# Kernel optimization log

Measured on AMD Instinct MI355X. Metric: run time of the kernel, lower is better.

The kernel has to match this reference:

```python
import jax, jax.numpy as jnp
import numpy as np

# irreps '32x0e + 32x1o + 16x2e': dims 32 (l=0), 96 (l=1, 32x3), 80 (l=2, 16x5) -> 208
MUL0, MUL1, MUL2 = 32, 32, 16
SC = 64  # scalar_channels
N_NODES, N_EDGES = 50000, 200000
FAN_IN = MUL0 * MUL0 + MUL1 * MUL1 + MUL2 * MUL2  # fully-connected path fan-in


def setup_inputs() -> dict:
    key = jax.random.key(0)
    ks = jax.random.split(key, 10)
    node_tensors = jax.random.normal(ks[0], (N_NODES, 208), dtype=jnp.float32)
    edge_index = jax.random.randint(ks[1], (2, N_EDGES), 0, N_NODES)
    # FullyConnectedTensorProduct path weights (mul1, mul2, mul_out)
    W0 = jax.random.normal(ks[2], (MUL0, MUL0, SC), dtype=jnp.float32)
    W1 = jax.random.normal(ks[3], (MUL1, MUL1, SC), dtype=jnp.float32)
    W2 = jax.random.normal(ks[4], (MUL2, MUL2, SC), dtype=jnp.float32)
    # MLP: Linear(64,32) -> SiLU -> Linear(32,1)
    A1 = jax.random.normal(ks[5], (SC, SC // 2), dtype=jnp.float32) / np.float32(np.sqrt(SC))
    b1 = jnp.zeros((SC // 2,), dtype=jnp.float32)
    A2 = jax.random.normal(ks[6], (SC // 2, 1), dtype=jnp.float32) / np.float32(np.sqrt(SC // 2))
    b2 = jnp.zeros((1,), dtype=jnp.float32)
    return {"node_tensors": node_tensors, "edge_index": edge_index,
            "W0": W0, "W1": W1, "W2": W2, "A1": A1, "b1": b1, "A2": A2, "b2": b2}


def _split_irreps(x):
    # x: [E, 208] -> scalars [E,32], vectors [E,32,3], rank-2 [E,16,5]
    s = x[:, :MUL0]
    v = x[:, MUL0:MUL0 + MUL1 * 3].reshape(-1, MUL1, 3)
    t = x[:, MUL0 + MUL1 * 3:].reshape(-1, MUL2, 5)
    return s, v, t


def reference(node_tensors, edge_index, W0, W1, W2, A1, b1, A2, b2):
    src, dst = edge_index[0], edge_index[1]
    x1 = node_tensors[src]  # [E, 208]
    x2 = node_tensors[dst]
    s1, v1, t1 = _split_irreps(x1)
    s2, v2, t2 = _split_irreps(x2)
    alpha = np.float32(1.0 / np.sqrt(FAN_IN))  # path normalization
    # l x l -> 0 Clebsch-Gordan: delta_{m1 m2} / sqrt(2l+1)
    e = alpha * (
        jnp.einsum('eu,ev,uvw->ew', s1, s2, W0)
        + jnp.einsum('eum,evm,uvw->ew', v1, v2, W1) / np.float32(np.sqrt(3.0))
        + jnp.einsum('eum,evm,uvw->ew', t1, t2, W2) / np.float32(np.sqrt(5.0))
    )  # [E, 64]
    h = jax.nn.silu(e @ A1 + b1)
    return (h @ A2 + b2)[:, 0]  # [E]
```

## Files before the change

kernel.cpp:

```cpp
#include <hip/hip_runtime.h>
#include <hip/hip_fp16.h>
#include <stdint.h>

#define N_EDGES 200000
#define N_NODES 50000
#define BM 32
#define NT 64

typedef _Float16 f16x8 __attribute__((ext_vector_type(8)));
typedef float f32x4 __attribute__((ext_vector_type(4)));

__global__ void prep_w(const float* __restrict__ W0, const float* __restrict__ W1,
                       const float* __restrict__ W2, uint16_t* __restrict__ wt) {
  int o = blockIdx.x * 256 + threadIdx.x;
  int T = o >> 11, r = o & 2047, w = r >> 5, kk = r & 31;
  int k = T * 32 + kk;
  const float AS = 1.0f / 48.0f;
  const float AV = AS * 0.57735026918962576f;
  const float AT = AS * 0.44721359549995794f;
  float val;
  if (k < 1024)      val = AS * W0[(k >> 5) * 2048 + (k & 31) * 64 + w];
  else if (k < 2048) { int k2 = k - 1024; val = AV * W1[(k2 >> 5) * 2048 + (k2 & 31) * 64 + w]; }
  else               { int k2 = k - 2048; val = AT * W2[(k2 >> 4) * 1024 + (k2 & 15) * 64 + w]; }
  __half h = __float2half(val);
  wt[o] = *reinterpret_cast<uint16_t*>(&h);
}

__global__ void prep_tables(const float* __restrict__ nt,
                            uint16_t* __restrict__ ta, uint16_t* __restrict__ tb) {
  long long o = (long long)blockIdx.x * 256 + threadIdx.x;
  if (o >= (long long)N_NODES * 296) return;
  int node = (int)(o / 296);
  int r = (int)(o - (long long)node * 296);
  const float* x = nt + (size_t)node * 208;
  float va = 0.f;
  if (r < 32) va = x[r];
  else if (r < 160) { int q = r - 32;  int u = q >> 2, m = q & 3;  if (m < 3) va = x[32 + u * 3 + m]; }
  else if (r < 288) { int q = r - 160; int u = q >> 3, m = q & 7;  if (m < 5) va = x[128 + u * 5 + m]; }
  __half ha = __float2half(va);
  ta[(size_t)node * 296 + r] = *reinterpret_cast<uint16_t*>(&ha);
  if (r < 216) {
    float vb = 0.f;
    if (r < 32) vb = x[r];
    else if (r < 128) { int q = r - 32;  int m = q >> 5, v = q & 31; vb = x[32 + v * 3 + m]; }
    else if (r < 208) { int q = r - 128; int m = q >> 4, v = q & 15; vb = x[128 + v * 5 + m]; }
    __half hb = __float2half(vb);
    tb[(size_t)node * 216 + r] = *reinterpret_cast<uint16_t*>(&hb);
  }
}

__device__ __forceinline__ __half2 bcast_half(uint32_t w, int sel) {
  uint32_t hv = sel ? (w >> 16) : (w & 0xffffu);
  hv |= hv << 16;
  union { uint32_t u; __half2 h; } cv; cv.u = hv;
  return cv.h;
}

#define LOADW(WRA, TEXPR)                                                       \
  { int Tc_ = (TEXPR);                                                          \
    _Pragma("unroll") for (int nf = 0; nf < 4; ++nf)                            \
      WRA[nf] = wtg4[Tc_ * 256 + nf * 64 + lo4]; }

#define MSTEPA(WRA, A)                                                          \
  _Pragma("unroll") for (int mf = 0; mf < 2; ++mf)                              \
  _Pragma("unroll") for (int nf = 0; nf < 4; ++nf)                              \
    acc[mf][nf] = __builtin_amdgcn_mfma_f32_16x16x32_f16(                       \
        (A)[mf], *(const f16x8*)&WRA[nf], acc[mf][nf], 0, 0, 0);

#define BUILD_SR(T_, A)                                                         \
  _Pragma("unroll") for (int mf = 0; mf < 2; ++mf) {                            \
    __half2 s1b2 = bcast_half(sS[mf][(T_) >> 1], (T_) & 1);                     \
    union { uint32_t u[4]; f16x8 v; } au_;                                      \
    _Pragma("unroll") for (int q = 0; q < 4; ++q) {                             \
      __half2 p = __hmul2(s1b2, ((const __half2*)&s2pk[mf])[q]);                \
      au_.u[q] = *(uint32_t*)&p;                                                \
    }                                                                           \
    (A)[mf] = au_.v;                                                            \
  }

#define BUILD_VR(UL, A)                                                         \
  _Pragma("unroll") for (int mf = 0; mf < 2; ++mf) {                            \
    __half2 va0 = bcast_half(vS[mf][(UL) * 2], 0);                              \
    __half2 va1 = bcast_half(vS[mf][(UL) * 2], 1);                              \
    __half2 va2 = bcast_half(vS[mf][(UL) * 2 + 1], 0);                          \
    union { uint32_t u[4]; f16x8 v; } au_;                                      \
    _Pragma("unroll") for (int q = 0; q < 4; ++q) {                             \
      __half2 p = __hmul2(va0, ((const __half2*)&v2pk[mf][0])[q]);              \
      p = __hfma2(va1, ((const __half2*)&v2pk[mf][1])[q], p);                   \
      p = __hfma2(va2, ((const __half2*)&v2pk[mf][2])[q], p);                   \
      au_.u[q] = *(uint32_t*)&p;                                                \
    }                                                                           \
    (A)[mf] = au_.v;                                                            \
  }

#define BUILD_TR(TT_, A)                                                        \
  _Pragma("unroll") for (int mm = 0; mm < 2; ++mm) {                            \
    __half2 tb0 = bcast_half(tS[mm][(TT_) * 4 + 0], 0);                         \
    __half2 tb1 = bcast_half(tS[mm][(TT_) * 4 + 0], 1);                         \
    __half2 tb2 = bcast_half(tS[mm][(TT_) * 4 + 1], 0);                         \
    __half2 tb3 = bcast_half(tS[mm][(TT_) * 4 + 1], 1);                         \
    __half2 tb4 = bcast_half(tS[mm][(TT_) * 4 + 2], 0);                         \
    union { uint32_t u[4]; f16x8 v; } au_;                                      \
    _Pragma("unroll") for (int q = 0; q < 4; ++q) {                             \
      __half2 p = __hmul2(tb0, ((const __half2*)&t2pk[mm][0])[q]);              \
      p = __hfma2(tb1, ((const __half2*)&t2pk[mm][1])[q], p);                   \
      p = __hfma2(tb2, ((const __half2*)&t2pk[mm][2])[q], p);                   \
      p = __hfma2(tb3, ((const __half2*)&t2pk[mm][3])[q], p);                   \
      p = __hfma2(tb4, ((const __half2*)&t2pk[mm][4])[q], p);                   \
      au_.u[q] = *(uint32_t*)&p;                                                \
    }                                                                           \
    (A)[mm] = au_.v;                                                            \
  }

#define RING_SR(WRA, T_)     { f16x8 a[2]; BUILD_SR(T_, a); MSTEPA(WRA, a); LOADW(WRA, (T_) + 4); }
#define RING_VR(WRA, UL, TB) { f16x8 a[2]; BUILD_VR(UL, a); MSTEPA(WRA, a); LOADW(WRA, (TB) + (UL) + 4); }
#define WRAPT(X) ((X) <= 71 ? (X) : (X) - 8)
#define RING_TR(WRA, TT_, TB){ f16x8 a[2]; BUILD_TR(TT_, a); MSTEPA(WRA, a); LOADW(WRA, WRAPT((TB) + (TT_) + 4)); }

__global__ __launch_bounds__(NT) void edge_main(
    const uint16_t* __restrict__ ta, const uint16_t* __restrict__ tbl,
    const int* __restrict__ ei, const uint16_t* __restrict__ wt,
    const float* __restrict__ A1, const float* __restrict__ b1,
    const float* __restrict__ A2, const float* __restrict__ b2,
    float* __restrict__ out)
{
  __shared__ alignas(16) float etile[32 * 68];
  const int tid = threadIdx.x;
  const int e0 = blockIdx.x * BM;
  const int lane = tid, c = lane & 15, g = lane >> 4;
  const int lo4 = c * 4 + g;

  const unsigned char* x1p[2];
  const unsigned char* tbp[2];
  #pragma unroll
  for (int mf = 0; mf < 2; ++mf) {
    int e = e0 + mf * 16 + c;
    int src = ei[e];
    int dst = ei[N_EDGES + e];
    x1p[mf] = (const unsigned char*)ta + (size_t)src * 592;
    tbp[mf] = (const unsigned char*)tbl + (size_t)dst * 432;
  }

  f32x4 acc[2][4];
  #pragma unroll
  for (int mf = 0; mf < 2; ++mf)
    #pragma unroll
    for (int nf = 0; nf < 4; ++nf) acc[mf][nf] = (f32x4){0.f, 0.f, 0.f, 0.f};

  const uint4* wtg4 = (const uint4*)wt;
  uint4 wr0[4], wr1[4], wr2[4], wr3[4];
  LOADW(wr0, 0); LOADW(wr1, 1); LOADW(wr2, 2); LOADW(wr3, 3);

  {
    uint4 s2pk[2];
    #pragma unroll
    for (int mf = 0; mf < 2; ++mf) s2pk[mf] = *(const uint4*)(tbp[mf] + g * 16);
    uint32_t sS[2][16];
    #pragma unroll
    for (int mf = 0; mf < 2; ++mf)
      #pragma unroll
      for (int i = 0; i < 4; ++i) {
        uint4 q_ = *(const uint4*)(x1p[mf] + i * 16);
        sS[mf][i * 4 + 0] = q_.x; sS[mf][i * 4 + 1] = q_.y;
        sS[mf][i * 4 + 2] = q_.z; sS[mf][i * 4 + 3] = q_.w;
      }
    #pragma unroll
    for (int T4 = 0; T4 < 8; ++T4) {
      RING_SR(wr0, T4 * 4 + 0); RING_SR(wr1, T4 * 4 + 1);
      RING_SR(wr2, T4 * 4 + 2); RING_SR(wr3, T4 * 4 + 3);
    }
  }

  {
    uint4 v2pk[2][3];
    #pragma unroll
    for (int mf = 0; mf < 2; ++mf)
      #pragma unroll
      for (int m3 = 0; m3 < 3; ++m3)
        v2pk[mf][m3] = *(const uint4*)(tbp[mf] + 64 + m3 * 64 + g * 16);
    for (int G = 0; G < 4; ++G) {
      uint32_t vS[2][16];
      #pragma unroll
      for (int mf = 0; mf < 2; ++mf)
        #pragma unroll
        for (int i = 0; i < 4; ++i) {
          uint4 q_ = *(const uint4*)(x1p[mf] + 64 + G * 64 + i * 16);
          vS[mf][i * 4 + 0] = q_.x; vS[mf][i * 4 + 1] = q_.y;
          vS[mf][i * 4 + 2] = q_.z; vS[mf][i * 4 + 3] = q_.w;
        }
      const int Tb = 32 + G * 8;
      RING_VR(wr0, 0, Tb); RING_VR(wr1, 1, Tb); RING_VR(wr2, 2, Tb); RING_VR(wr3, 3, Tb);
      RING_VR(wr0, 4, Tb); RING_VR(wr1, 5, Tb); RING_VR(wr2, 6, Tb); RING_VR(wr3, 7, Tb);
    }
  }

  {
    uint4 t2pk[2][5];
    #pragma unroll
    for (int mm = 0; mm < 2; ++mm)
      #pragma unroll
      for (int m5 = 0; m5 < 5; ++m5)
        t2pk[mm][m5] = *(const uint4*)(tbp[mm] + 256 + m5 * 32 + (g & 1) * 16);
    const int gh16 = (g >> 1) * 16;
    #pragma unroll
    for (int H = 0; H < 2; ++H) {
      uint32_t tS[2][16];
      #pragma unroll
      for (int mm = 0; mm < 2; ++mm)
        #pragma unroll
        for (int i = 0; i < 4; ++i) {
          uint4 q_ = *(const uint4*)(x1p[mm] + 320 + gh16 + H * 128 + i * 32);
          tS[mm][i * 4 + 0] = q_.x; tS[mm][i * 4 + 1] = q_.y;
          tS[mm][i * 4 + 2] = q_.z; tS[mm][i * 4 + 3] = q_.w;
        }
      const int Tb = 64 + H * 4;
      RING_TR(wr0, 0, Tb); RING_TR(wr1, 1, Tb); RING_TR(wr2, 2, Tb); RING_TR(wr3, 3, Tb);
    }
  }

  #pragma unroll
  for (int mf = 0; mf < 2; ++mf)
    #pragma unroll
    for (int nf = 0; nf < 4; ++nf)
      #pragma unroll
      for (int rr = 0; rr < 4; ++rr)
        etile[(mf * 16 + g * 4 + rr) * 68 + nf * 16 + c] = acc[mf][nf][rr];
  __syncthreads();

  {
    int el = lane >> 1, jh = lane & 1;
    const float* er = etile + (size_t)el * 68;
    float hacc[16];
    #pragma unroll
    for (int j = 0; j < 16; ++j) hacc[j] = b1[jh * 16 + j];
    for (int w4 = 0; w4 < 16; ++w4) {
      float4 ea = *(const float4*)(er + w4 * 4);
      #pragma unroll
      for (int q2 = 0; q2 < 4; ++q2) {
        float ev = (&ea.x)[q2];
        int w = w4 * 4 + q2;
        float4 a0 = *(const float4*)(A1 + w * 32 + jh * 16);
        float4 a1 = *(const float4*)(A1 + w * 32 + jh * 16 + 4);
        float4 a2 = *(const float4*)(A1 + w * 32 + jh * 16 + 8);
        float4 a3 = *(const float4*)(A1 + w * 32 + jh * 16 + 12);
        hacc[0]  += ev * a0.x; hacc[1]  += ev * a0.y; hacc[2]  += ev * a0.z; hacc[3]  += ev * a0.w;
        hacc[4]  += ev * a1.x; hacc[5]  += ev * a1.y; hacc[6]  += ev * a1.z; hacc[7]  += ev * a1.w;
        hacc[8]  += ev * a2.x; hacc[9]  += ev * a2.y; hacc[10] += ev * a2.z; hacc[11] += ev * a2.w;
        hacc[12] += ev * a3.x; hacc[13] += ev * a3.y; hacc[14] += ev * a3.z; hacc[15] += ev * a3.w;
      }
    }
    float o = 0.f;
    #pragma unroll
    for (int j = 0; j < 16; ++j) {
      float z = hacc[j];
      o += (z / (1.f + __expf(-z))) * A2[jh * 16 + j];
    }
    o += __shfl_xor(o, 1);
    int e = e0 + el;
    if (jh == 0 && e < N_EDGES) out[e] = o + b2[0];
  }
}

extern "C" void kernel_launch(void* const* d_in, const int* in_sizes, int n_in,
                              void* d_out, int out_size, void* d_ws, size_t ws_size,
                              hipStream_t stream) {
  const float* nt = (const float*)d_in[0];
  const int*   ei = (const int*)d_in[1];
  const float* W0 = (const float*)d_in[2];
  const float* W1 = (const float*)d_in[3];
  const float* W2 = (const float*)d_in[4];
  const float* A1 = (const float*)d_in[5];
  const float* b1 = (const float*)d_in[6];
  const float* A2 = (const float*)d_in[7];
  const float* b2 = (const float*)d_in[8];
  float* out = (float*)d_out;

  uint16_t* wt = (uint16_t*)d_ws;
  uint16_t* ta = (uint16_t*)((char*)d_ws + 294912);
  uint16_t* tb = (uint16_t*)((char*)d_ws + 294912 + (size_t)N_NODES * 592);

  prep_w<<<576, 256, 0, stream>>>(W0, W1, W2, wt);
  {
    long long tot = (long long)N_NODES * 296;
    int blocks = (int)((tot + 255) / 256);
    prep_tables<<<blocks, 256, 0, stream>>>(nt, ta, tb);
  }
  edge_main<<<N_EDGES / BM, NT, 0, stream>>>(ta, tb, ei, wt, A1, b1, A2, b2, out);
}
```

Measured before the change: 226.6 us.

## Stage shared fp16 weights through LDS with async global-to-LDS ring buffer

```diff
diff --git a/kernel.cpp b/kernel.cpp
--- a/kernel.cpp
+++ b/kernel.cpp
@@ -4,8 +4,9 @@
 
 #define N_EDGES 200000
 #define N_NODES 50000
-#define BM 32
-#define NT 64
+#define BM 256
+#define NT 512
+#define GTOT 36
 
 typedef _Float16 f16x8 __attribute__((ext_vector_type(8)));
 typedef float f32x4 __attribute__((ext_vector_type(4)));
@@ -49,6 +50,12 @@
   }
 }
 
+__device__ __forceinline__ void gload16(const void* g, void* l) {
+  __builtin_amdgcn_global_load_lds(
+      (const __attribute__((address_space(1))) void*)g,
+      (__attribute__((address_space(3))) void*)l, 16, 0, 0);
+}
+
 __device__ __forceinline__ __half2 bcast_half(uint32_t w, int sel) {
   uint32_t hv = sel ? (w >> 16) : (w & 0xffffu);
   hv |= hv << 16;
@@ -56,10 +63,23 @@
   return cv.h;
 }
 
-#define LOADW(WRA, TEXPR)                                                       \
-  { int Tc_ = (TEXPR);                                                          \
+#define STAGEW(G)                                                               \
+  if ((G) < GTOT) {                                                             \
+    gload16((const char*)wt + (size_t)(G) * 8192 + tid * 16,                    \
+            (void*)(smem + ((G) & 3) * 8192 + (tid >> 6) * 1024));              \
+  }
+#define WAITV(G)                                                                \
+  do {                                                                          \
+    if ((G) >= GTOT - 1)      asm volatile("s_waitcnt vmcnt(0)" ::: "memory");  \
+    else if ((G) == GTOT - 2) asm volatile("s_waitcnt vmcnt(1)" ::: "memory");  \
+    else                      asm volatile("s_waitcnt vmcnt(2)" ::: "memory");  \
+  } while (0)
+#define BARRIER() asm volatile("s_barrier" ::: "memory")
+
+#define LDSW(WRA, G, TL)                                                        \
+  { const uint4* wb_ = (const uint4*)(smem + ((G) & 3) * 8192 + (TL) * 4096);   \
     _Pragma("unroll") for (int nf = 0; nf < 4; ++nf)                            \
-      WRA[nf] = wtg4[Tc_ * 256 + nf * 64 + lo4]; }
+      WRA[nf] = wb_[nf * 64 + lo4]; }
 
 #define MSTEPA(WRA, A)                                                          \
   _Pragma("unroll") for (int mf = 0; mf < 2; ++mf)                              \
@@ -112,29 +132,26 @@
     (A)[mm] = au_.v;                                                            \
   }
 
-#define RING_SR(WRA, T_)     { f16x8 a[2]; BUILD_SR(T_, a); MSTEPA(WRA, a); LOADW(WRA, (T_) + 4); }
-#define RING_VR(WRA, UL, TB) { f16x8 a[2]; BUILD_VR(UL, a); MSTEPA(WRA, a); LOADW(WRA, (TB) + (UL) + 4); }
-#define WRAPT(X) ((X) <= 71 ? (X) : (X) - 8)
-#define RING_TR(WRA, TT_, TB){ f16x8 a[2]; BUILD_TR(TT_, a); MSTEPA(WRA, a); LOADW(WRA, WRAPT((TB) + (TT_) + 4)); }
-
-__global__ __launch_bounds__(NT) void edge_main(
+__global__ __launch_bounds__(NT, 2) void edge_main(
     const uint16_t* __restrict__ ta, const uint16_t* __restrict__ tbl,
     const int* __restrict__ ei, const uint16_t* __restrict__ wt,
     const float* __restrict__ A1, const float* __restrict__ b1,
     const float* __restrict__ A2, const float* __restrict__ b2,
     float* __restrict__ out)
 {
-  __shared__ alignas(16) float etile[32 * 68];
+  __shared__ alignas(16) unsigned char smem[69632];
   const int tid = threadIdx.x;
   const int e0 = blockIdx.x * BM;
-  const int lane = tid, c = lane & 15, g = lane >> 4;
+  const int lane = tid & 63, c = lane & 15, g = lane >> 4;
+  const int wv = tid >> 6;
   const int lo4 = c * 4 + g;
 
   const unsigned char* x1p[2];
   const unsigned char* tbp[2];
   #pragma unroll
   for (int mf = 0; mf < 2; ++mf) {
-    int e = e0 + mf * 16 + c;
+    int e = e0 + wv * 32 + mf * 16 + c;
+    if (e > N_EDGES - 1) e = N_EDGES - 1;
     int src = ei[e];
     int dst = ei[N_EDGES + e];
     x1p[mf] = (const unsigned char*)ta + (size_t)src * 592;
@@ -147,9 +164,8 @@
     #pragma unroll
     for (int nf = 0; nf < 4; ++nf) acc[mf][nf] = (f32x4){0.f, 0.f, 0.f, 0.f};
 
-  const uint4* wtg4 = (const uint4*)wt;
-  uint4 wr0[4], wr1[4], wr2[4], wr3[4];
-  LOADW(wr0, 0); LOADW(wr1, 1); LOADW(wr2, 2); LOADW(wr3, 3);
+  STAGEW(0);
+  STAGEW(1);
 
   {
     uint4 s2pk[2];
@@ -165,9 +181,14 @@
         sS[mf][i * 4 + 2] = q_.z; sS[mf][i * 4 + 3] = q_.w;
       }
     #pragma unroll
-    for (int T4 = 0; T4 < 8; ++T4) {
-      RING_SR(wr0, T4 * 4 + 0); RING_SR(wr1, T4 * 4 + 1);
-      RING_SR(wr2, T4 * 4 + 2); RING_SR(wr3, T4 * 4 + 3);
+    for (int q = 0; q < 16; ++q) {
+      STAGEW(q + 2);
+      WAITV(q);
+      BARRIER();
+      uint4 wrA[4], wrB[4];
+      LDSW(wrA, q, 0); LDSW(wrB, q, 1);
+      { f16x8 a[2]; BUILD_SR(2 * q, a);     MSTEPA(wrA, a); }
+      { f16x8 a[2]; BUILD_SR(2 * q + 1, a); MSTEPA(wrB, a); }
     }
   }
 
@@ -178,19 +199,27 @@
       #pragma unroll
       for (int m3 = 0; m3 < 3; ++m3)
         v2pk[mf][m3] = *(const uint4*)(tbp[mf] + 64 + m3 * 64 + g * 16);
-    for (int G = 0; G < 4; ++G) {
-      uint32_t vS[2][16];
-      #pragma unroll
-      for (int mf = 0; mf < 2; ++mf)
+    uint32_t vS[2][16];
+    #pragma unroll
+    for (int q = 0; q < 16; ++q) {
+      if ((q & 3) == 0) {
+        const int G4 = q >> 2;
         #pragma unroll
-        for (int i = 0; i < 4; ++i) {
-          uint4 q_ = *(const uint4*)(x1p[mf] + 64 + G * 64 + i * 16);
-          vS[mf][i * 4 + 0] = q_.x; vS[mf][i * 4 + 1] = q_.y;
-          vS[mf][i * 4 + 2] = q_.z; vS[mf][i * 4 + 3] = q_.w;
-        }
-      const int Tb = 32 + G * 8;
-      RING_VR(wr0, 0, Tb); RING_VR(wr1, 1, Tb); RING_VR(wr2, 2, Tb); RING_VR(wr3, 3, Tb);
-      RING_VR(wr0, 4, Tb); RING_VR(wr1, 5, Tb); RING_VR(wr2, 6, Tb); RING_VR(wr3, 7, Tb);
+        for (int mf = 0; mf < 2; ++mf)
+          #pragma unroll
+          for (int i = 0; i < 4; ++i) {
+            uint4 q_ = *(const uint4*)(x1p[mf] + 64 + G4 * 64 + i * 16);
+            vS[mf][i * 4 + 0] = q_.x; vS[mf][i * 4 + 1] = q_.y;
+            vS[mf][i * 4 + 2] = q_.z; vS[mf][i * 4 + 3] = q_.w;
+          }
+      }
+      STAGEW(16 + q + 2);
+      WAITV(16 + q);
+      BARRIER();
+      uint4 wrA[4], wrB[4];
+      LDSW(wrA, 16 + q, 0); LDSW(wrB, 16 + q, 1);
+      { f16x8 a[2]; BUILD_VR((2 * q) & 7, a);     MSTEPA(wrA, a); }
+      { f16x8 a[2]; BUILD_VR((2 * q + 1) & 7, a); MSTEPA(wrB, a); }
     }
   }
 
@@ -202,33 +231,44 @@
       for (int m5 = 0; m5 < 5; ++m5)
         t2pk[mm][m5] = *(const uint4*)(tbp[mm] + 256 + m5 * 32 + (g & 1) * 16);
     const int gh16 = (g >> 1) * 16;
-    #pragma unroll
-    for (int H = 0; H < 2; ++H) {
-      uint32_t tS[2][16];
-      #pragma unroll
-      for (int mm = 0; mm < 2; ++mm)
+    uint32_t tS[2][16];
+    #pragma unroll
+    for (int q = 0; q < 4; ++q) {
+      if ((q & 1) == 0) {
+        const int H = q >> 1;
         #pragma unroll
-        for (int i = 0; i < 4; ++i) {
-          uint4 q_ = *(const uint4*)(x1p[mm] + 320 + gh16 + H * 128 + i * 32);
-          tS[mm][i * 4 + 0] = q_.x; tS[mm][i * 4 + 1] = q_.y;
-          tS[mm][i * 4 + 2] = q_.z; tS[mm][i * 4 + 3] = q_.w;
-        }
-      const int Tb = 64 + H * 4;
-      RING_TR(wr0, 0, Tb); RING_TR(wr1, 1, Tb); RING_TR(wr2, 2, Tb); RING_TR(wr3, 3, Tb);
-    }
-  }
-
+        for (int mm = 0; mm < 2; ++mm)
+          #pragma unroll
+          for (int i = 0; i < 4; ++i) {
+            uint4 q_ = *(const uint4*)(x1p[mm] + 320 + gh16 + H * 128 + i * 32);
+            tS[mm][i * 4 + 0] = q_.x; tS[mm][i * 4 + 1] = q_.y;
+            tS[mm][i * 4 + 2] = q_.z; tS[mm][i * 4 + 3] = q_.w;
+          }
+      }
+      STAGEW(32 + q + 2);
+      WAITV(32 + q);
+      BARRIER();
+      uint4 wrA[4], wrB[4];
+      LDSW(wrA, 32 + q, 0); LDSW(wrB, 32 + q, 1);
+      { f16x8 a[2]; BUILD_TR((2 * q) & 3, a);     MSTEPA(wrA, a); }
+      { f16x8 a[2]; BUILD_TR((2 * q + 1) & 3, a); MSTEPA(wrB, a); }
+    }
+  }
+
+  BARRIER();
+  float* etile = (float*)smem;
   #pragma unroll
   for (int mf = 0; mf < 2; ++mf)
     #pragma unroll
     for (int nf = 0; nf < 4; ++nf)
       #pragma unroll
       for (int rr = 0; rr < 4; ++rr)
-        etile[(mf * 16 + g * 4 + rr) * 68 + nf * 16 + c] = acc[mf][nf][rr];
+        etile[(size_t)(wv * 32 + mf * 16 + g * 4 + rr) * 68 + nf * 16 + c] =
+            acc[mf][nf][rr];
   __syncthreads();
 
   {
-    int el = lane >> 1, jh = lane & 1;
+    int el = tid >> 1, jh = tid & 1;
     const float* er = etile + (size_t)el * 68;
     float hacc[16];
     #pragma unroll
@@ -285,5 +325,5 @@
     int blocks = (int)((tot + 255) / 256);
     prep_tables<<<blocks, 256, 0, stream>>>(nt, ta, tb);
   }
-  edge_main<<<N_EDGES / BM, NT, 0, stream>>>(ta, tb, ei, wt, A1, b1, A2, b2, out);
-}
+  edge_main<<<(N_EDGES + BM - 1) / BM, NT, 0, stream>>>(ta, tb, ei, wt, A1, b1, A2, b2, out);
+}
```

Result: slower. 231.6 us (+2.2%).
